# Kernel tuning notes

Hardware: AMD Instinct MI355X
Metric: run time of the kernel (lower is better)

## Reference

```python
import jax, jax.numpy as jnp
import numpy as np

D_MODEL = 1024
NUM_HEADS = 16
HEAD_DIM = D_MODEL // NUM_HEADS


def setup_inputs() -> dict:
    key = jax.random.key(0)
    ks = jax.random.split(key, 9)
    B, S = 4, 2048
    bound = 1.0 / np.sqrt(D_MODEL)  # nn.Linear default init range
    def lin(kw, kb):
        W = jax.random.uniform(kw, (D_MODEL, D_MODEL), jnp.float32, -bound, bound)
        b = jax.random.uniform(kb, (D_MODEL,), jnp.float32, -bound, bound)
        return W, b
    Wq, bq = lin(ks[0], ks[1])
    Wk, bk = lin(ks[2], ks[3])
    Wv, bv = lin(ks[4], ks[5])
    Wo, bo = lin(ks[6], ks[7])
    x = jax.random.normal(ks[8], (B, S, D_MODEL), jnp.float32)
    return {"x": x, "Wq": Wq, "bq": bq, "Wk": Wk, "bk": bk,
            "Wv": Wv, "bv": bv, "Wo": Wo, "bo": bo}


def reference(x, Wq, bq, Wk, bk, Wv, bv, Wo, bo):
    B, S, _ = x.shape
    scale = 1.0 / np.sqrt(HEAD_DIM)
    # projections; torch Linear is x @ W.T + b; here W stored as [in, out]-style [d,d] already transposed
    def split_heads(t):
        return t.reshape(B, S, NUM_HEADS, HEAD_DIM).transpose(0, 2, 1, 3)  # [B,H,S,Dh]
    q = split_heads(x @ Wq + bq)
    k = split_heads(x @ Wk + bk)
    v = split_heads(x @ Wv + bv)
    scores = jnp.einsum('bhqd,bhkd->bhqk', q, k) * scale  # [B,H,S,S]
    attn = jax.nn.softmax(scores, axis=-1)
    out = jnp.einsum('bhqk,bhkd->bhqd', attn, v)  # [B,H,S,Dh]
    out = out.transpose(0, 2, 1, 3).reshape(B, S, D_MODEL)
    return out @ Wo + bo
```

## Files before the change

kernel.cpp:

```cpp
#include <hip/hip_runtime.h>
#include <hip/hip_bf16.h>

typedef __attribute__((ext_vector_type(8))) short short8;
typedef __attribute__((ext_vector_type(4))) float f32x4;
typedef __attribute__((ext_vector_type(16))) float f32x16;

#define MFMA16(a, b, c) __builtin_amdgcn_mfma_f32_16x16x32_bf16((a), (b), (c), 0, 0, 0)
#define MFMA32(a, b, c) __builtin_amdgcn_mfma_f32_32x32x16_bf16((a), (b), (c), 0, 0, 0)

__device__ __forceinline__ void gload_lds16(const void* g, void* l) {
  __builtin_amdgcn_global_load_lds(
      (const __attribute__((address_space(1))) unsigned int*)g,
      (__attribute__((address_space(3))) unsigned int*)l, 16, 0, 0);
}

__global__ __launch_bounds__(256) void cvt_x(const float* __restrict__ x,
                                             __hip_bfloat16* __restrict__ xb) {
  size_t i = ((size_t)blockIdx.x * 256 + threadIdx.x) * 8;
  float4 a = *(const float4*)(x + i);
  float4 b = *(const float4*)(x + i + 4);
  struct alignas(16) B8 { __hip_bfloat16 h[8]; } o;
  o.h[0] = __float2bfloat16(a.x); o.h[1] = __float2bfloat16(a.y);
  o.h[2] = __float2bfloat16(a.z); o.h[3] = __float2bfloat16(a.w);
  o.h[4] = __float2bfloat16(b.x); o.h[5] = __float2bfloat16(b.y);
  o.h[6] = __float2bfloat16(b.z); o.h[7] = __float2bfloat16(b.w);
  *(B8*)(xb + i) = o;
}

__global__ __launch_bounds__(256) void trans_w(const float* __restrict__ W0,
                                               const float* __restrict__ W1,
                                               const float* __restrict__ W2,
                                               const float* __restrict__ W3,
                                               __hip_bfloat16* __restrict__ Wt) {
  const int which = blockIdx.z;
  const float* W = (which == 0) ? W0 : (which == 1) ? W1 : (which == 2) ? W2 : W3;
  __hip_bfloat16* O = Wt + (size_t)which * 1024 * 1024;
  __shared__ __hip_bfloat16 lds[64][65];
  const int k0 = blockIdx.y * 64, n0 = blockIdx.x * 64;
#pragma unroll
  for (int i = 0; i < 16; ++i) {
    int idx = threadIdx.x + i * 256;
    int r = idx >> 6, c = idx & 63;
    lds[r][c] = __float2bfloat16(W[(size_t)(k0 + r) * 1024 + n0 + c]);
  }
  __syncthreads();
#pragma unroll
  for (int i = 0; i < 16; ++i) {
    int idx = threadIdx.x + i * 256;
    int r = idx >> 6, c = idx & 63;
    O[(size_t)(n0 + r) * 1024 + k0 + c] = lds[c][r];
  }
}

__global__ __launch_bounds__(512) void gemm_qkv(const __hip_bfloat16* __restrict__ A,
                                                const __hip_bfloat16* __restrict__ Wt,
                                                const float* __restrict__ bq,
                                                const float* __restrict__ bk,
                                                const float* __restrict__ bv,
                                                __hip_bfloat16* __restrict__ Qb,
                                                __hip_bfloat16* __restrict__ Kb,
                                                __hip_bfloat16* __restrict__ Vtb) {
  __shared__ __hip_bfloat16 Asm[2][256 * 64];
  __shared__ __hip_bfloat16 Bsm[2][256 * 64];
  const int t = threadIdx.x;
  const int lane = t & 63, w = t >> 6;
  const int l15 = lane & 15, g = lane >> 4;
  const int wm = (w >> 2) * 128;
  const int wn = (w & 3) * 64;
  const int bid = (blockIdx.x & 7) * 48 + (blockIdx.x >> 3);
  const int mb0 = (bid / 12) * 256;
  const int nbg = (bid % 12) * 256;
  const int which = nbg >> 10;
  const int nb0 = nbg & 1023;
  const __hip_bfloat16* Bt = Wt + (size_t)which * 1048576;
  const float* bias = (which == 0) ? bq : (which == 1) ? bk : bv;
  f32x4 acc[8][4] = {};

  const int srow = t >> 3;
  const int ssl = (t & 7) ^ (srow & 7);
  const __hip_bfloat16* Ags = A + (size_t)(mb0 + srow) * 1024 + ssl * 8;
  const __hip_bfloat16* Bgs = Bt + (size_t)(nb0 + srow) * 1024 + ssl * 8;

#define STAGE_TILE(bufi, k0n)                                          \
  do {                                                                 \
    _Pragma("unroll") for (int uu = 0; uu < 4; ++uu) {                 \
      gload_lds16(Ags + (size_t)uu * 65536 + (k0n),                    \
                  (char*)&Asm[bufi][0] + uu * 8192 + t * 16);          \
      gload_lds16(Bgs + (size_t)uu * 65536 + (k0n),                    \
                  (char*)&Bsm[bufi][0] + uu * 8192 + t * 16);          \
    }                                                                  \
  } while (0)

#define QUAD(cA, cB, mh, nh)                                                     \
  do {                                                                           \
    short8 af[4][2], bf[2][2];                                                   \
    _Pragma("unroll") for (int mi = 0; mi < 4; ++mi) {                           \
      int row = wm + ((mh) * 4 + mi) * 16 + l15;                                 \
      _Pragma("unroll") for (int kk = 0; kk < 2; ++kk)                           \
        af[mi][kk] = *(const short8*)((cA) + row * 128 +                         \
                                      (((kk * 4 + g) ^ (row & 7)) * 16));        \
    }                                                                            \
    _Pragma("unroll") for (int ni = 0; ni < 2; ++ni) {                           \
      int row = wn + ((nh) * 2 + ni) * 16 + l15;                                 \
      _Pragma("unroll") for (int kk = 0; kk < 2; ++kk)                           \
        bf[ni][kk] = *(const short8*)((cB) + row * 128 +                         \
                                      (((kk * 4 + g) ^ (row & 7)) * 16));        \
    }                                                                            \
    __builtin_amdgcn_s_barrier();                                                \
    _Pragma("unroll") for (int mi = 0; mi < 4; ++mi)                             \
      _Pragma("unroll") for (int ni = 0; ni < 2; ++ni)                           \
        _Pragma("unroll") for (int kk = 0; kk < 2; ++kk)                         \
          acc[(mh) * 4 + mi][(nh) * 2 + ni] =                                    \
              MFMA16(af[mi][kk], bf[ni][kk], acc[(mh) * 4 + mi][(nh) * 2 + ni]); \
    __builtin_amdgcn_s_barrier();                                                \
  } while (0)

  STAGE_TILE(0, 0);
  asm volatile("s_waitcnt vmcnt(0)" ::: "memory");
  __builtin_amdgcn_s_barrier();

  for (int u = 0; u < 16; ++u) {
    const int cur = u & 1;
    const char* cA = (const char*)&Asm[cur][0];
    const char* cB = (const char*)&Bsm[cur][0];
    if (u < 15) STAGE_TILE(cur ^ 1, (u + 1) * 64);
    QUAD(cA, cB, 0, 0);
    QUAD(cA, cB, 0, 1);
    QUAD(cA, cB, 1, 0);
    QUAD(cA, cB, 1, 1);
    asm volatile("s_waitcnt vmcnt(0)" ::: "memory");
    __builtin_amdgcn_s_barrier();
  }
#undef STAGE_TILE
#undef QUAD

#pragma unroll
  for (int ni = 0; ni < 4; ++ni) {
    int col = nb0 + wn + ni * 16 + l15;
    float bvv = bias[col];
#pragma unroll
    for (int mi = 0; mi < 8; ++mi) {
#pragma unroll
      for (int r = 0; r < 4; ++r) {
        int row = mb0 + wm + mi * 16 + g * 4 + r;
        __hip_bfloat16 hv = __float2bfloat16(acc[mi][ni][r] + bvv);
        if (which == 2) {
          int bb = row >> 11, s = row & 2047;
          int sp = (s & ~12) | ((s & 4) << 1) | ((s & 8) >> 1);
          Vtb[((size_t)(bb * 1024 + col) << 11) + sp] = hv;
        } else {
          __hip_bfloat16* O = which ? Kb : Qb;
          O[(size_t)row * 1024 + col] = hv;
        }
      }
    }
  }
}

__global__ __launch_bounds__(256) void gemm_o(const __hip_bfloat16* __restrict__ A,
                                              const __hip_bfloat16* __restrict__ Bt,
                                              const float* __restrict__ bias,
                                              float* __restrict__ outp) {
  __shared__ __hip_bfloat16 Asm[3][128 * 32];
  __shared__ __hip_bfloat16 Bsm[3][128 * 32];
  const int t = threadIdx.x;
  const int lane = t & 63, w = t >> 6, g = lane >> 4;
  const int bid = (blockIdx.x & 7) * 64 + (blockIdx.x >> 3);
  const int mb0 = (bid / 8) * 128;
  const int nb0 = (bid % 8) * 128;
  const int wr = (w >> 1) * 64, wc = (w & 1) * 64;
  f32x4 acc[4][4] = {};

  const int srow0 = t >> 2;
  const int ssl0 = (t & 3) ^ ((srow0 >> 1) & 3);
  const int srow1 = (t >> 2) + 64;
  const int ssl1 = (t & 3) ^ ((srow1 >> 1) & 3);
  const __hip_bfloat16* Ag0 = A + (size_t)(mb0 + srow0) * 1024 + ssl0 * 8;
  const __hip_bfloat16* Ag1 = A + (size_t)(mb0 + srow1) * 1024 + ssl1 * 8;
  const __hip_bfloat16* Bg0 = Bt + (size_t)(nb0 + srow0) * 1024 + ssl0 * 8;
  const __hip_bfloat16* Bg1 = Bt + (size_t)(nb0 + srow1) * 1024 + ssl1 * 8;
  const int ldst = (t * 16);
  char* wA0 = (char*)&Asm[0][0]; char* wB0 = (char*)&Bsm[0][0];
  char* wA1 = (char*)&Asm[1][0]; char* wB1 = (char*)&Bsm[1][0];
  char* wA2 = (char*)&Asm[2][0]; char* wB2 = (char*)&Bsm[2][0];

#define STAGE_TO(pA, pB, k0n)                                \
  do {                                                       \
    gload_lds16(Ag0 + (k0n), pA + ldst);                     \
    gload_lds16(Ag1 + (k0n), pA + 4096 + ldst);              \
    gload_lds16(Bg0 + (k0n), pB + ldst);                     \
    gload_lds16(Bg1 + (k0n), pB + 4096 + ldst);              \
  } while (0)

#define COMPUTE_FROM(rA, rB)                                                     \
  do {                                                                           \
    short8 a[4], b[4];                                                           \
    _Pragma("unroll") for (int m = 0; m < 4; ++m) {                              \
      int row = wr + m * 16 + (lane & 15);                                       \
      a[m] = *(const short8*)(rA + row * 64 + ((g ^ ((row >> 1) & 3)) * 16));    \
    }                                                                            \
    _Pragma("unroll") for (int n = 0; n < 4; ++n) {                              \
      int row = wc + n * 16 + (lane & 15);                                       \
      b[n] = *(const short8*)(rB + row * 64 + ((g ^ ((row >> 1) & 3)) * 16));    \
    }                                                                            \
    _Pragma("unroll") for (int m = 0; m < 4; ++m)                                \
      _Pragma("unroll") for (int n = 0; n < 4; ++n)                              \
        acc[m][n] = MFMA16(a[m], b[n], acc[m][n]);                               \
  } while (0)

  STAGE_TO(wA0, wB0, 0);
  STAGE_TO(wA1, wB1, 32);
  asm volatile("s_waitcnt vmcnt(4)" ::: "memory");
  __syncthreads();

  for (int u = 0; u < 30; ++u) {
    COMPUTE_FROM(wA0, wB0);
    STAGE_TO(wA2, wB2, (u + 2) * 32);
    asm volatile("s_waitcnt vmcnt(4)" ::: "memory");
    __syncthreads();
    char* tA = wA0; wA0 = wA1; wA1 = wA2; wA2 = tA;
    char* tB = wB0; wB0 = wB1; wB1 = wB2; wB2 = tB;
  }
  COMPUTE_FROM(wA0, wB0);
  asm volatile("s_waitcnt vmcnt(0)" ::: "memory");
  __syncthreads();
  COMPUTE_FROM(wA1, wB1);

#undef STAGE_TO
#undef COMPUTE_FROM

#pragma unroll
  for (int n = 0; n < 4; ++n) {
    int col = nb0 + wc + n * 16 + (lane & 15);
    float bvv = bias[col];
#pragma unroll
    for (int m = 0; m < 4; ++m)
#pragma unroll
      for (int r = 0; r < 4; ++r) {
        int row = mb0 + wr + m * 16 + g * 4 + r;
        outp[(size_t)row * 1024 + col] = acc[m][n][r] + bvv;
      }
  }
}

__global__ __launch_bounds__(256, 2) void attn_fwd8(const __hip_bfloat16* __restrict__ Q,
                                                    const __hip_bfloat16* __restrict__ Kg,
                                                    const __hip_bfloat16* __restrict__ Vt,
                                                    __hip_bfloat16* __restrict__ ctx) {
  __shared__ __hip_bfloat16 Ksm[2][64 * 64];
  __shared__ __hip_bfloat16 Vsm[2][64 * 64];
  const int t = threadIdx.x, lane = t & 63, w = t >> 6;
  const int l31 = lane & 31, hi = lane >> 5;
  const int bid = (blockIdx.x & 7) * 64 + (blockIdx.x >> 3);
  const int bh = bid >> 3, qt = bid & 7;
  const int b = bh >> 4, h = bh & 15;
  const int qA = qt * 256 + w * 64 + l31;

  short8 qfA[4], qfB[4];
  {
    const __hip_bfloat16* qp = Q + ((size_t)(b * 2048 + qA)) * 1024 + h * 64 + hi * 8;
#pragma unroll
    for (int c = 0; c < 4; ++c) qfA[c] = *(const short8*)(qp + 16 * c);
    qp += 32 * 1024;
#pragma unroll
    for (int c = 0; c < 4; ++c) qfB[c] = *(const short8*)(qp + 16 * c);
  }
  const __hip_bfloat16* Kbh = Kg + (size_t)b * 2048 * 1024 + h * 64;
  const __hip_bfloat16* Vbh = Vt + (size_t)(b * 16 + h) * 64 * 2048;

  const int srow = t >> 3;
  const int sslot = t & 7;

#define STAGE(buf, ktn)                                                          \
  do {                                                                           \
    _Pragma("unroll") for (int i = 0; i < 2; ++i) {                              \
      int row = i * 32 + srow;                                                   \
      int sl = sslot ^ (row & 7);                                                \
      gload_lds16(Kbh + (size_t)((ktn) + row) * 1024 + sl * 8,                   \
                  (char*)&Ksm[buf][0] + i * 4096 + w * 1024);                    \
      gload_lds16(Vbh + (size_t)row * 2048 + (ktn) + sl * 8,                     \
                  (char*)&Vsm[buf][0] + i * 4096 + w * 1024);                    \
    }                                                                            \
  } while (0)

  f32x16 otA0 = {}, otA1 = {}, otB0 = {}, otB1 = {};
  float lsA0 = 0.f, lsA1 = 0.f, lsB0 = 0.f, lsB1 = 0.f;
  const float CL = 0.18033688011112042f;
  const float NEG = -43.28085122666891f;

  STAGE(0, 0);
  asm volatile("s_waitcnt vmcnt(0)" ::: "memory");
  __syncthreads();

  for (int kt = 0; kt < 2048; kt += 64) {
    const int cur = (kt >> 6) & 1;
    if (kt + 64 < 2048) STAGE(cur ^ 1, kt + 64);

    const char* Kb0 = (const char*)&Ksm[cur][0];
    const char* Vb0 = (const char*)&Vsm[cur][0];

    f32x16 sA0 = {}, sA1 = {}, sB0 = {}, sB1 = {};
    {
      short8 kf[2][4];
#pragma unroll
      for (int s = 0; s < 2; ++s)
#pragma unroll
        for (int c = 0; c < 4; ++c) {
          int row = s * 32 + l31;
          kf[s][c] = *(const short8*)(Kb0 + row * 128 + (((hi + 2 * c) ^ (row & 7)) * 16));
        }
#pragma unroll
      for (int c = 0; c < 4; ++c) {
        sA0 = MFMA32(kf[0][c], qfA[c], sA0);
        sA1 = MFMA32(kf[1][c], qfA[c], sA1);
        sB0 = MFMA32(kf[0][c], qfB[c], sB0);
        sB1 = MFMA32(kf[1][c], qfB[c], sB1);
      }
    }

    short8 vf[2][4];
#pragma unroll
    for (int dt = 0; dt < 2; ++dt)
#pragma unroll
      for (int c = 0; c < 4; ++c) {
        int row = dt * 32 + l31;
        vf[dt][c] = *(const short8*)(Vb0 + row * 128 + (((hi + 2 * c) ^ (row & 7)) * 16));
      }

    {
      unsigned ua[16];
#pragma unroll
      for (int n = 0; n < 8; ++n) {
        float a0 = __builtin_fmaf(sA0[2 * n], CL, NEG);
        float a1 = __builtin_fmaf(sA0[2 * n + 1], CL, NEG);
        float e0, e1;
        asm("v_exp_f32 %0, %1" : "=v"(e0) : "v"(a0));
        asm("v_exp_f32 %0, %1" : "=v"(e1) : "v"(a1));
        lsA0 += e0; lsA1 += e1;
        asm("v_cvt_pk_bf16_f32 %0, %1, %2" : "=v"(ua[n]) : "v"(e0), "v"(e1));
      }
#pragma unroll
      for (int n = 0; n < 8; ++n) {
        float a0 = __builtin_fmaf(sA1[2 * n], CL, NEG);
        float a1 = __builtin_fmaf(sA1[2 * n + 1], CL, NEG);
        float e0, e1;
        asm("v_exp_f32 %0, %1" : "=v"(e0) : "v"(a0));
        asm("v_exp_f32 %0, %1" : "=v"(e1) : "v"(a1));
        lsA0 += e0; lsA1 += e1;
        asm("v_cvt_pk_bf16_f32 %0, %1, %2" : "=v"(ua[8 + n]) : "v"(e0), "v"(e1));
      }
#pragma unroll
      for (int c = 0; c < 4; ++c) {
        union { unsigned u[4]; short8 s8; } pb;
        pb.u[0] = ua[4 * c]; pb.u[1] = ua[4 * c + 1];
        pb.u[2] = ua[4 * c + 2]; pb.u[3] = ua[4 * c + 3];
        otA0 = MFMA32(vf[0][c], pb.s8, otA0);
        otA1 = MFMA32(vf[1][c], pb.s8, otA1);
      }
    }

    {
      unsigned ub[16];
#pragma unroll
      for (int n = 0; n < 8; ++n) {
        float a0 = __builtin_fmaf(sB0[2 * n], CL, NEG);
        float a1 = __builtin_fmaf(sB0[2 * n + 1], CL, NEG);
        float e0, e1;
        asm("v_exp_f32 %0, %1" : "=v"(e0) : "v"(a0));
        asm("v_exp_f32 %0, %1" : "=v"(e1) : "v"(a1));
        lsB0 += e0; lsB1 += e1;
        asm("v_cvt_pk_bf16_f32 %0, %1, %2" : "=v"(ub[n]) : "v"(e0), "v"(e1));
      }
#pragma unroll
      for (int n = 0; n < 8; ++n) {
        float a0 = __builtin_fmaf(sB1[2 * n], CL, NEG);
        float a1 = __builtin_fmaf(sB1[2 * n + 1], CL, NEG);
        float e0, e1;
        asm("v_exp_f32 %0, %1" : "=v"(e0) : "v"(a0));
        asm("v_exp_f32 %0, %1" : "=v"(e1) : "v"(a1));
        lsB0 += e0; lsB1 += e1;
        asm("v_cvt_pk_bf16_f32 %0, %1, %2" : "=v"(ub[8 + n]) : "v"(e0), "v"(e1));
      }
#pragma unroll
      for (int c = 0; c < 4; ++c) {
        union { unsigned u[4]; short8 s8; } pb;
        pb.u[0] = ub[4 * c]; pb.u[1] = ub[4 * c + 1];
        pb.u[2] = ub[4 * c + 2]; pb.u[3] = ub[4 * c + 3];
        otB0 = MFMA32(vf[0][c], pb.s8, otB0);
        otB1 = MFMA32(vf[1][c], pb.s8, otB1);
      }
    }

    asm volatile("s_waitcnt vmcnt(0)" ::: "memory");
    __syncthreads();
  }
#undef STAGE

  float lsumA = lsA0 + lsA1;
  lsumA += __shfl_xor(lsumA, 32);
  float invA = 1.0f / lsumA;
  float lsumB = lsB0 + lsB1;
  lsumB += __shfl_xor(lsumB, 32);
  float invB = 1.0f / lsumB;

  {
    __hip_bfloat16* op = ctx + ((size_t)(b * 2048 + qA)) * 1024 + h * 64 + 4 * hi;
#pragma unroll
    for (int dt = 0; dt < 2; ++dt) {
#pragma unroll
      for (int g = 0; g < 4; ++g) {
        struct alignas(8) H4 { __hip_bfloat16 x[4]; } o4;
#pragma unroll
        for (int e = 0; e < 4; ++e)
          o4.x[e] = __float2bfloat16((dt ? otA1[4 * g + e] : otA0[4 * g + e]) * invA);
        *(H4*)(op + 32 * dt + 8 * g) = o4;
      }
    }
    op += 32 * 1024;
#pragma unroll
    for (int dt = 0; dt < 2; ++dt) {
#pragma unroll
      for (int g = 0; g < 4; ++g) {
        struct alignas(8) H4 { __hip_bfloat16 x[4]; } o4;
#pragma unroll
        for (int e = 0; e < 4; ++e)
          o4.x[e] = __float2bfloat16((dt ? otB1[4 * g + e] : otB0[4 * g + e]) * invB);
        *(H4*)(op + 32 * dt + 8 * g) = o4;
      }
    }
  }
}

extern "C" void kernel_launch(void* const* d_in, const int* in_sizes, int n_in,
                              void* d_out, int out_size, void* d_ws, size_t ws_size,
                              hipStream_t stream) {
  (void)in_sizes; (void)n_in; (void)out_size; (void)ws_size;
  const float* x  = (const float*)d_in[0];
  const float* Wq = (const float*)d_in[1];
  const float* bq = (const float*)d_in[2];
  const float* Wk = (const float*)d_in[3];
  const float* bk = (const float*)d_in[4];
  const float* Wv = (const float*)d_in[5];
  const float* bv = (const float*)d_in[6];
  const float* Wo = (const float*)d_in[7];
  const float* bo = (const float*)d_in[8];
  float* out = (float*)d_out;

  __hip_bfloat16* ws  = (__hip_bfloat16*)d_ws;
  __hip_bfloat16* xb  = ws;
  __hip_bfloat16* Wt  = xb + 8388608;
  __hip_bfloat16* Qb  = Wt + 4194304;
  __hip_bfloat16* Kb  = Qb + 8388608;
  __hip_bfloat16* Vtb = Kb + 8388608;
  __hip_bfloat16* ctx = xb;

  cvt_x<<<4096, 256, 0, stream>>>(x, xb);
  trans_w<<<dim3(16, 16, 4), 256, 0, stream>>>(Wq, Wk, Wv, Wo, Wt);
  gemm_qkv<<<384, 512, 0, stream>>>(xb, Wt, bq, bk, bv, Qb, Kb, Vtb);
  attn_fwd8<<<512, 256, 0, stream>>>(Qb, Kb, Vtb, ctx);
  gemm_o<<<512, 256, 0, stream>>>(ctx, Wt + 3145728, bo, out);
}
```

Before: 236.8 us.

## Restructure QKV GEMM pipeline to prefetch two tiles ahead with fragment reuse

The QKV projection GEMM now issues global-to-LDS loads two K-tiles ahead into the same double buffer. It waits with vmcnt(8) instead of draining all loads each iteration, and the new loads go out only after the current buffer has been read. A and B fragments are reused across the four quadrant MFMA groups, which cuts LDS reads. The launch bounds ask for two blocks per CU. In the output GEMM, __syncthreads is replaced by a raw s_barrier plus a compiler fence. This raises load/compute overlap and lowers LDS traffic, but fragment reuse adds register pressure, and the raw barriers make correctness depend on the hand-placed waitcnts.

```diff
diff --git a/kernel.cpp b/kernel.cpp
--- a/kernel.cpp
+++ b/kernel.cpp
@@ -13,6 +13,8 @@
       (const __attribute__((address_space(1))) unsigned int*)g,
       (__attribute__((address_space(3))) unsigned int*)l, 16, 0, 0);
 }
+
+#define RAW_BAR() __builtin_amdgcn_s_barrier()
 
 __global__ __launch_bounds__(256) void cvt_x(const float* __restrict__ x,
                                              __hip_bfloat16* __restrict__ xb) {
@@ -52,14 +54,14 @@
   }
 }
 
-__global__ __launch_bounds__(512) void gemm_qkv(const __hip_bfloat16* __restrict__ A,
-                                                const __hip_bfloat16* __restrict__ Wt,
-                                                const float* __restrict__ bq,
-                                                const float* __restrict__ bk,
-                                                const float* __restrict__ bv,
-                                                __hip_bfloat16* __restrict__ Qb,
-                                                __hip_bfloat16* __restrict__ Kb,
-                                                __hip_bfloat16* __restrict__ Vtb) {
+__global__ __launch_bounds__(512, 2) void gemm_qkv(const __hip_bfloat16* __restrict__ A,
+                                                   const __hip_bfloat16* __restrict__ Wt,
+                                                   const float* __restrict__ bq,
+                                                   const float* __restrict__ bk,
+                                                   const float* __restrict__ bv,
+                                                   __hip_bfloat16* __restrict__ Qb,
+                                                   __hip_bfloat16* __restrict__ Kb,
+                                                   __hip_bfloat16* __restrict__ Vtb) {
   __shared__ __hip_bfloat16 Asm[2][256 * 64];
   __shared__ __hip_bfloat16 Bsm[2][256 * 64];
   const int t = threadIdx.x;
@@ -76,62 +78,92 @@
   const float* bias = (which == 0) ? bq : (which == 1) ? bk : bv;
   f32x4 acc[8][4] = {};
 
-  const int srow = t >> 3;
-  const int ssl = (t & 7) ^ (srow & 7);
-  const __hip_bfloat16* Ags = A + (size_t)(mb0 + srow) * 1024 + ssl * 8;
-  const __hip_bfloat16* Bgs = Bt + (size_t)(nb0 + srow) * 1024 + ssl * 8;
-
-#define STAGE_TILE(bufi, k0n)                                          \
-  do {                                                                 \
-    _Pragma("unroll") for (int uu = 0; uu < 4; ++uu) {                 \
-      gload_lds16(Ags + (size_t)uu * 65536 + (k0n),                    \
-                  (char*)&Asm[bufi][0] + uu * 8192 + t * 16);          \
-      gload_lds16(Bgs + (size_t)uu * 65536 + (k0n),                    \
-                  (char*)&Bsm[bufi][0] + uu * 8192 + t * 16);          \
-    }                                                                  \
+  const int tp0 = t, tp1 = 512 + t;
+  const int r0 = tp0 >> 3, s0 = (tp0 & 7) ^ (r0 & 7);
+  const int r1 = tp1 >> 3, s1 = (tp1 & 7) ^ (r1 & 7);
+  const __hip_bfloat16* Ag[2][2];
+  const __hip_bfloat16* Bg[2][2];
+  Ag[0][0] = A + (size_t)(mb0 + r0) * 1024 + s0 * 8;
+  Ag[0][1] = A + (size_t)(mb0 + r1) * 1024 + s1 * 8;
+  Ag[1][0] = A + (size_t)(mb0 + 128 + r0) * 1024 + s0 * 8;
+  Ag[1][1] = A + (size_t)(mb0 + 128 + r1) * 1024 + s1 * 8;
+  Bg[0][0] = Bt + (size_t)(nb0 + r0) * 1024 + s0 * 8;
+  Bg[0][1] = Bt + (size_t)(nb0 + r1) * 1024 + s1 * 8;
+  Bg[1][0] = Bt + (size_t)(nb0 + 128 + r0) * 1024 + s0 * 8;
+  Bg[1][1] = Bt + (size_t)(nb0 + 128 + r1) * 1024 + s1 * 8;
+
+#define STAGE_KT(pA, pB, k0n)                                           \
+  do {                                                                  \
+    gload_lds16(Ag[0][0] + (k0n), (pA) + tp0 * 16);                     \
+    gload_lds16(Ag[0][1] + (k0n), (pA) + tp1 * 16);                     \
+    gload_lds16(Ag[1][0] + (k0n), (pA) + 16384 + tp0 * 16);             \
+    gload_lds16(Ag[1][1] + (k0n), (pA) + 16384 + tp1 * 16);             \
+    gload_lds16(Bg[0][0] + (k0n), (pB) + tp0 * 16);                     \
+    gload_lds16(Bg[0][1] + (k0n), (pB) + tp1 * 16);                     \
+    gload_lds16(Bg[1][0] + (k0n), (pB) + 16384 + tp0 * 16);             \
+    gload_lds16(Bg[1][1] + (k0n), (pB) + 16384 + tp1 * 16);             \
   } while (0)
 
-#define QUAD(cA, cB, mh, nh)                                                     \
-  do {                                                                           \
-    short8 af[4][2], bf[2][2];                                                   \
-    _Pragma("unroll") for (int mi = 0; mi < 4; ++mi) {                           \
-      int row = wm + ((mh) * 4 + mi) * 16 + l15;                                 \
-      _Pragma("unroll") for (int kk = 0; kk < 2; ++kk)                           \
-        af[mi][kk] = *(const short8*)((cA) + row * 128 +                         \
-                                      (((kk * 4 + g) ^ (row & 7)) * 16));        \
-    }                                                                            \
-    _Pragma("unroll") for (int ni = 0; ni < 2; ++ni) {                           \
-      int row = wn + ((nh) * 2 + ni) * 16 + l15;                                 \
-      _Pragma("unroll") for (int kk = 0; kk < 2; ++kk)                           \
-        bf[ni][kk] = *(const short8*)((cB) + row * 128 +                         \
-                                      (((kk * 4 + g) ^ (row & 7)) * 16));        \
-    }                                                                            \
-    __builtin_amdgcn_s_barrier();                                                \
-    _Pragma("unroll") for (int mi = 0; mi < 4; ++mi)                             \
-      _Pragma("unroll") for (int ni = 0; ni < 2; ++ni)                           \
-        _Pragma("unroll") for (int kk = 0; kk < 2; ++kk)                         \
-          acc[(mh) * 4 + mi][(nh) * 2 + ni] =                                    \
-              MFMA16(af[mi][kk], bf[ni][kk], acc[(mh) * 4 + mi][(nh) * 2 + ni]); \
-    __builtin_amdgcn_s_barrier();                                                \
-  } while (0)
-
-  STAGE_TILE(0, 0);
-  asm volatile("s_waitcnt vmcnt(0)" ::: "memory");
-  __builtin_amdgcn_s_barrier();
+#define RD_A(dst, base, mi0)                                                       \
+  _Pragma("unroll") for (int mi = 0; mi < 4; ++mi)                                 \
+    _Pragma("unroll") for (int kk = 0; kk < 2; ++kk) {                             \
+      int row = wm + ((mi0) + mi) * 16 + l15;                                      \
+      dst[mi][kk] = *(const short8*)((base) + row * 128 +                          \
+                                     (((kk * 4 + g) ^ (row & 7)) * 16));           \
+    }
+#define RD_B(dst, base, ni0)                                                       \
+  _Pragma("unroll") for (int ni = 0; ni < 2; ++ni)                                 \
+    _Pragma("unroll") for (int kk = 0; kk < 2; ++kk) {                             \
+      int row = wn + ((ni0) + ni) * 16 + l15;                                      \
+      dst[ni][kk] = *(const short8*)((base) + row * 128 +                          \
+                                     (((kk * 4 + g) ^ (row & 7)) * 16));           \
+    }
+#define QUAD(af, bf, mi0, ni0)                                                     \
+  _Pragma("unroll") for (int mi = 0; mi < 4; ++mi)                                 \
+    _Pragma("unroll") for (int ni = 0; ni < 2; ++ni)                               \
+      _Pragma("unroll") for (int kk = 0; kk < 2; ++kk)                             \
+        acc[(mi0) + mi][(ni0) + ni] =                                              \
+            MFMA16(af[mi][kk], bf[ni][kk], acc[(mi0) + mi][(ni0) + ni]);
+
+  char* A0 = (char*)&Asm[0][0]; char* B0 = (char*)&Bsm[0][0];
+  char* A1 = (char*)&Asm[1][0]; char* B1p = (char*)&Bsm[1][0];
+
+  STAGE_KT(A0, B0, 0);
+  STAGE_KT(A1, B1p, 64);
+  asm volatile("s_waitcnt vmcnt(8)" ::: "memory");
+  RAW_BAR();
 
   for (int u = 0; u < 16; ++u) {
-    const int cur = u & 1;
-    const char* cA = (const char*)&Asm[cur][0];
-    const char* cB = (const char*)&Bsm[cur][0];
-    if (u < 15) STAGE_TILE(cur ^ 1, (u + 1) * 64);
-    QUAD(cA, cB, 0, 0);
-    QUAD(cA, cB, 0, 1);
-    QUAD(cA, cB, 1, 0);
-    QUAD(cA, cB, 1, 1);
-    asm volatile("s_waitcnt vmcnt(0)" ::: "memory");
-    __builtin_amdgcn_s_barrier();
-  }
-#undef STAGE_TILE
+    char* rA = (u & 1) ? A1 : A0;
+    char* rB = (u & 1) ? B1p : B0;
+
+    short8 af0[4][2], af1[4][2], bf0[2][2], bf1[2][2];
+    RD_A(af0, rA, 0);
+    RD_B(bf0, rB, 0);
+    RAW_BAR();
+    QUAD(af0, bf0, 0, 0);
+    RAW_BAR();
+    RD_B(bf1, rB, 2);
+    RAW_BAR();
+    QUAD(af0, bf1, 0, 2);
+    RAW_BAR();
+    RD_A(af1, rA, 4);
+    RAW_BAR();
+    QUAD(af1, bf0, 4, 0);
+    RAW_BAR();
+    if (u <= 13) STAGE_KT(rA, rB, (u + 2) * 64);
+    RAW_BAR();
+    QUAD(af1, bf1, 4, 2);
+    if (u <= 13) {
+      asm volatile("s_waitcnt vmcnt(8)" ::: "memory");
+    } else if (u == 14) {
+      asm volatile("s_waitcnt vmcnt(0)" ::: "memory");
+    }
+    RAW_BAR();
+  }
+#undef STAGE_KT
+#undef RD_A
+#undef RD_B
 #undef QUAD
 
 #pragma unroll
@@ -217,13 +249,15 @@
     COMPUTE_FROM(wA0, wB0);
     STAGE_TO(wA2, wB2, (u + 2) * 32);
     asm volatile("s_waitcnt vmcnt(4)" ::: "memory");
-    __syncthreads();
+    __builtin_amdgcn_s_barrier();
+    asm volatile("" ::: "memory");
     char* tA = wA0; wA0 = wA1; wA1 = wA2; wA2 = tA;
     char* tB = wB0; wB0 = wB1; wB1 = wB2; wB2 = tB;
   }
   COMPUTE_FROM(wA0, wB0);
   asm volatile("s_waitcnt vmcnt(0)" ::: "memory");
-  __syncthreads();
+  __builtin_amdgcn_s_barrier();
+  asm volatile("" ::: "memory");
   COMPUTE_FROM(wA1, wB1);
 
 #undef STAGE_TO
```

New measurement: 223.2 us. 5.7% less time.
